# Kernel tuning notes

Hardware: AMD Instinct MI355X
Metric: run time of the kernel (lower is better)

Reference implementation:

```python
import math
import jax, jax.numpy as jnp
from jax import lax
import numpy as np

D_MODEL, D_STATE, D_CONV, EXPAND = 96, 16, 3, 2
D_INNER = EXPAND * D_MODEL            # 192
DT_RANK = math.ceil(D_MODEL / 16)     # 6
B_, H_, W_ = 2, 64, 64


def setup_inputs() -> dict:
    key = jax.random.key(0)
    ks = jax.random.split(key, 8)
    x = jax.random.normal(ks[0], (B_, H_, W_, D_MODEL), jnp.float32)
    in_proj_w = jax.random.normal(ks[1], (2 * D_INNER, D_MODEL), jnp.float32) * (D_MODEL ** -0.5)
    conv_w = jax.random.normal(ks[2], (D_INNER, 1, D_CONV, D_CONV), jnp.float32) * 0.1  # depthwise OIHW
    conv_b = jax.random.normal(ks[3], (D_INNER,), jnp.float32) * 0.1
    x_proj_weight = jax.random.normal(ks[4], (4, DT_RANK + 2 * D_STATE, D_INNER), jnp.float32) * (D_INNER ** -0.5)
    dt_init_std = DT_RANK ** -0.5
    dt_projs_weight = jax.random.uniform(ks[5], (4, D_INNER, DT_RANK), jnp.float32, -dt_init_std, dt_init_std)
    dt = jnp.exp(jax.random.uniform(ks[6], (4, D_INNER), jnp.float32) * (math.log(0.1) - math.log(0.001)) + math.log(0.001))
    dt = jnp.clip(dt, 1e-4, None)
    dt_projs_bias = dt + jnp.log(-jnp.expm1(-dt))  # inverse softplus init
    A_logs = jnp.log(jnp.tile(jnp.arange(1.0, D_STATE + 1.0, dtype=jnp.float32), (4 * D_INNER, 1)))  # (4*D, N)
    Ds = jnp.ones((4 * D_INNER,), jnp.float32)
    out_norm_w = jnp.ones((D_INNER,), jnp.float32)
    out_norm_b = jnp.zeros((D_INNER,), jnp.float32)
    out_proj_w = jax.random.normal(ks[7], (D_MODEL, D_INNER), jnp.float32) * (D_INNER ** -0.5)
    return dict(x=x, in_proj_w=in_proj_w, conv_w=conv_w, conv_b=conv_b,
                x_proj_weight=x_proj_weight, dt_projs_weight=dt_projs_weight,
                dt_projs_bias=dt_projs_bias, A_logs=A_logs, Ds=Ds,
                out_norm_w=out_norm_w, out_norm_b=out_norm_b, out_proj_w=out_proj_w)


def _ss2d(x, in_proj_w, conv_w, conv_b, x_proj_weight, dt_projs_weight,
          dt_projs_bias, A_logs, Ds, out_norm_w, out_norm_b, out_proj_w):
    B, H, W, C = x.shape
    K = 4
    d_inner = conv_w.shape[0]
    d_state = A_logs.shape[1]
    dt_rank = dt_projs_weight.shape[2]
    L = H * W

    # in_proj + split into x / gate z
    xz = jnp.einsum('bhwc,ec->bhwe', x, in_proj_w)
    xi, z = jnp.split(xz, 2, axis=-1)

    # depthwise 3x3 conv (padding=1) + SiLU, channels-first
    xc = jnp.transpose(xi, (0, 3, 1, 2))  # B,D,H,W
    xc = lax.conv_general_dilated(xc, conv_w, (1, 1), 'SAME',
                                  feature_group_count=d_inner,
                                  dimension_numbers=('NCHW', 'OIHW', 'NCHW'))
    xc = jax.nn.silu(xc + conv_b[None, :, None, None])

    # 4 scan directions: row-major, col-major, and their reverses
    x_hw = xc.reshape(B, d_inner, L)
    x_wh = jnp.transpose(xc, (0, 1, 3, 2)).reshape(B, d_inner, L)
    x_hwwh = jnp.stack([x_hw, x_wh], axis=1)                        # B,2,D,L
    xs = jnp.concatenate([x_hwwh, jnp.flip(x_hwwh, axis=-1)], axis=1)  # B,K,D,L

    x_dbl = jnp.einsum('bkdl,kcd->bkcl', xs, x_proj_weight)
    dts, Bs, Cs = jnp.split(x_dbl, [dt_rank, dt_rank + d_state], axis=2)
    dts = jnp.einsum('bkrl,kdr->bkdl', dts, dt_projs_weight)
    delta = jax.nn.softplus(dts + dt_projs_bias[None, :, :, None])  # B,K,D,L
    A = -jnp.exp(A_logs).reshape(K, d_inner, d_state)               # K,D,N

    # selective scan over L (serial recurrence)
    d_s = jnp.moveaxis(delta, -1, 0)  # L,B,K,D
    u_s = jnp.moveaxis(xs, -1, 0)     # L,B,K,D
    B_s = jnp.moveaxis(Bs, -1, 0)     # L,B,K,N
    C_s = jnp.moveaxis(Cs, -1, 0)     # L,B,K,N

    def step(h, inp):
        d_t, u_t, Bt, Ct = inp
        dA = jnp.exp(d_t[..., None] * A)                       # B,K,D,N
        h = h * dA + (d_t * u_t)[..., None] * Bt[:, :, None, :]
        y = jnp.einsum('bkdn,bkn->bkd', h, Ct)
        return h, y

    h0 = jnp.zeros((B, K, d_inner, d_state), jnp.float32)
    _, ys = lax.scan(step, h0, (d_s, u_s, B_s, C_s))  # ys: L,B,K,D
    ys = jnp.moveaxis(ys, 0, -1)                      # B,K,D,L
    out_y = ys + xs * Ds.reshape(K, d_inner)[None, :, :, None]

    # merge directions back to row-major layout
    inv_y = jnp.flip(out_y[:, 2:4], axis=-1)
    wh_y = jnp.transpose(out_y[:, 1].reshape(B, d_inner, W, H), (0, 1, 3, 2)).reshape(B, d_inner, L)
    invwh_y = jnp.transpose(inv_y[:, 1].reshape(B, d_inner, W, H), (0, 1, 3, 2)).reshape(B, d_inner, L)
    y = out_y[:, 0] + inv_y[:, 0] + wh_y + invwh_y    # B,D,L

    y = jnp.transpose(y, (0, 2, 1)).reshape(B, H, W, d_inner)
    mu = y.mean(-1, keepdims=True)
    var = y.var(-1, keepdims=True)
    y = (y - mu) * lax.rsqrt(var + 1e-5) * out_norm_w + out_norm_b
    y = y * jax.nn.silu(z)
    return jnp.einsum('bhwd,cd->bhwc', y, out_proj_w)


def reference(x, in_proj_w, conv_w, conv_b, x_proj_weight, dt_projs_weight,
              dt_projs_bias, A_logs, Ds, out_norm_w, out_norm_b, out_proj_w):
    return _ss2d(x, in_proj_w, conv_w, conv_b, x_proj_weight, dt_projs_weight,
                 dt_projs_bias, A_logs, Ds, out_norm_w, out_norm_b, out_proj_w)
```

## Files before the change

### kernel.cpp

```cpp
#include <hip/hip_runtime.h>
#include <math.h>

#define DMODEL 96
#define DIN    192
#define NST    16
#define RK     6
#define KDIR   4
#define LLEN   4096
#define BB     2
#define BP_TOT 8192
#define SCH    128
#define TCH    32

__global__ __launch_bounds__(192) void k_inproj(const float* __restrict__ x,
                                                const float* __restrict__ Wp,
                                                float* __restrict__ xi,
                                                float* __restrict__ z)
{
    __shared__ float xs[8 * 96];
    const int t  = threadIdx.x;
    const int p0 = blockIdx.x * 8;
    for (int idx = t; idx < 768; idx += 192)
        xs[idx] = x[(size_t)p0 * 96 + idx];
    __syncthreads();

    float acc0[8], acc1[8];
    #pragma unroll
    for (int i = 0; i < 8; ++i) { acc0[i] = 0.f; acc1[i] = 0.f; }
    const float* w0p = Wp + (size_t)t * 96;
    const float* w1p = Wp + (size_t)(t + 192) * 96;
    for (int k = 0; k < 96; k += 4) {
        float4 w0 = *(const float4*)(w0p + k);
        float4 w1 = *(const float4*)(w1p + k);
        #pragma unroll
        for (int p = 0; p < 8; ++p) {
            float4 xv = *(const float4*)&xs[p * 96 + k];
            acc0[p] = fmaf(w0.x, xv.x, fmaf(w0.y, xv.y, fmaf(w0.z, xv.z, fmaf(w0.w, xv.w, acc0[p]))));
            acc1[p] = fmaf(w1.x, xv.x, fmaf(w1.y, xv.y, fmaf(w1.z, xv.z, fmaf(w1.w, xv.w, acc1[p]))));
        }
    }
    #pragma unroll
    for (int p = 0; p < 8; ++p) {
        xi[(size_t)(p0 + p) * 192 + t] = acc0[p];
        z [(size_t)(p0 + p) * 192 + t] = acc1[p];
    }
}

__device__ __forceinline__ int inv_perm(int kd, int p)
{
    if (kd == 0) return p;
    if (kd == 1) return ((p & 63) << 6) | (p >> 6);
    if (kd == 2) return 4095 - p;
    return 4095 - (((p & 63) << 6) | (p >> 6));
}

__device__ __forceinline__ int perm_pos(int k, int l)
{
    if (k == 0) return l;
    if (k == 1) return ((l & 63) << 6) | (l >> 6);
    if (k == 2) return 4095 - l;
    int lr = 4095 - l;
    return ((lr & 63) << 6) | (lr >> 6);
}

__device__ __forceinline__ float softplus_fast(float x)
{
    float r = __logf(1.f + __expf(x));
    return (x > 15.f) ? x : r;
}

__device__ __forceinline__ void pow_chain(float e1, float* aa)
{
    float e2 = e1 * e1, e4 = e2 * e2, e8 = e4 * e4, e16 = e8 * e8;
    float e3 = e2 * e1, e5 = e4 * e1, e6 = e4 * e2, e7 = e4 * e3;
    aa[0] = e1;  aa[1] = e2;  aa[2] = e3;  aa[3] = e4;
    aa[4] = e5;  aa[5] = e6;  aa[6] = e7;  aa[7] = e8;
    aa[8] = e8 * e1;  aa[9] = e8 * e2;  aa[10] = e8 * e3;  aa[11] = e8 * e4;
    aa[12] = e8 * e5; aa[13] = e8 * e6; aa[14] = e8 * e7;  aa[15] = e16;
}

__device__ __forceinline__ int sm_remap(int c)
{
    return (c < 6) ? (32 + c) : (c - 6);
}

__global__ __launch_bounds__(192) void k_convxdbl(const float* __restrict__ xi,
                                                  const float* __restrict__ cw,
                                                  const float* __restrict__ cb,
                                                  const float* __restrict__ xpw,
                                                  float* __restrict__ xc,
                                                  float* __restrict__ xdk)
{
    __shared__ float xs[8 * 192];
    const int t   = threadIdx.x;
    const int p0  = blockIdx.x * 8;
    const int b   = p0 >> 12;
    const int pp0 = p0 & 4095;
    const int row = pp0 >> 6, c0 = pp0 & 63;

    float w9[9];
    #pragma unroll
    for (int i = 0; i < 9; ++i) w9[i] = cw[t * 9 + i];
    const float cbias = cb[t];

    float xv[3][10];
    #pragma unroll
    for (int ky = 0; ky < 3; ++ky) {
        int rr = row + ky - 1;
        #pragma unroll
        for (int kx = 0; kx < 10; ++kx) {
            int cc = c0 + kx - 1;
            float v = 0.f;
            if (rr >= 0 && rr < 64 && cc >= 0 && cc < 64)
                v = xi[((size_t)b * 4096 + rr * 64 + cc) * 192 + t];
            xv[ky][kx] = v;
        }
    }
    #pragma unroll
    for (int p = 0; p < 8; ++p) {
        float s = cbias;
        #pragma unroll
        for (int ky = 0; ky < 3; ++ky)
            #pragma unroll
            for (int kx = 0; kx < 3; ++kx)
                s = fmaf(xv[ky][p + kx], w9[ky * 3 + kx], s);
        float sv = s * (1.f / (1.f + __expf(-s)));
        xc[(size_t)(p0 + p) * 192 + t] = sv;
        xs[p * 192 + t] = sv;
    }
    __syncthreads();
    if (t >= 152) return;

    const int kd = t / 38, r = t % 38;
    float acc[8];
    #pragma unroll
    for (int i = 0; i < 8; ++i) acc[i] = 0.f;
    const float* wr = xpw + (size_t)t * 192;
    for (int k = 0; k < 192; k += 4) {
        float4 w = *(const float4*)(wr + k);
        #pragma unroll
        for (int p = 0; p < 8; ++p) {
            float4 x4 = *(const float4*)&xs[p * 192 + k];
            acc[p] = fmaf(w.x, x4.x, fmaf(w.y, x4.y, fmaf(w.z, x4.z, fmaf(w.w, x4.w, acc[p]))));
        }
    }
    #pragma unroll
    for (int p = 0; p < 8; ++p) {
        int pp = pp0 + p;
        int l  = inv_perm(kd, pp);
        xdk[((size_t)(b * 4 + kd) * 4096 + l) * 38 + r] = acc[p];
    }
}

__global__ __launch_bounds__(192) void k_scan1(const float* __restrict__ xc,
                                               const float* __restrict__ xdk,
                                               const float* __restrict__ dtw,
                                               const float* __restrict__ dtb,
                                               const float* __restrict__ Alog,
                                               float* __restrict__ hend,
                                               float* __restrict__ prodA)
{
    __shared__ float sm[TCH * 40];
    const int t   = threadIdx.x;
    const int blk = blockIdx.x;
    const int s = blk & (SCH - 1), k = (blk >> 7) & 3, b = blk >> 9;
    const int kd = k * 192 + t;
    const int l0 = s * TCH;

    const float* src = xdk + ((size_t)(b * 4 + k) * 4096 + l0) * 38;
    for (int idx = t; idx < TCH * 38; idx += 192) {
        int st = idx / 38, c = idx % 38;
        sm[st * 40 + sm_remap(c)] = src[idx];
    }

    const float A0 = -__expf(Alog[kd * 16]);
    bool fast = true;
    #pragma unroll
    for (int n = 1; n < 16; ++n) {
        float An = -__expf(Alog[kd * 16 + n]);
        fast = fast && (fabsf(An - (float)(n + 1) * A0) <= 1e-3f * fabsf(An));
    }
    float wdt[6];
    #pragma unroll
    for (int r = 0; r < 6; ++r) wdt[r] = dtw[kd * 6 + r];
    const float bias = dtb[kd];

    float h[16];
    #pragma unroll
    for (int n = 0; n < 16; ++n) h[n] = 0.f;
    float cd = 0.f;

    const float* xcb = xc + (size_t)b * 4096 * 192;
    int allfast = __syncthreads_and((int)fast);

    int p_cur = perm_pos(k, l0);
    float u = xcb[(size_t)p_cur * 192 + t];

    if (allfast) {
        for (int g0 = 0; g0 < TCH; g0 += 8) {
            float e18[8], dl8[8];
            #pragma unroll
            for (int j = 0; j < 8; ++j) {
                const float* r = &sm[(g0 + j) * 40];
                float4 dq = *(const float4*)(r + 32);
                float xv = bias + dq.x * wdt[0] + dq.y * wdt[1] + dq.z * wdt[2]
                                + dq.w * wdt[3] + r[36] * wdt[4] + r[37] * wdt[5];
                float delta = softplus_fast(xv);
                dl8[j] = delta;
                e18[j] = __expf(delta * A0);
            }
            #pragma unroll
            for (int j = 0; j < 8; ++j) {
                int st = g0 + j;
                int p_next = (st + 1 < TCH) ? perm_pos(k, l0 + st + 1) : p_cur;
                float u_next = xcb[(size_t)p_next * 192 + t];
                const float* r = &sm[st * 40];
                cd += dl8[j];
                float du = dl8[j] * u;
                float aa[16];
                pow_chain(e18[j], aa);
                float4 b0 = *(const float4*)(r),      b1 = *(const float4*)(r + 4);
                float4 b2 = *(const float4*)(r + 8),  b3 = *(const float4*)(r + 12);
                float bv[16] = {b0.x, b0.y, b0.z, b0.w, b1.x, b1.y, b1.z, b1.w,
                                b2.x, b2.y, b2.z, b2.w, b3.x, b3.y, b3.z, b3.w};
                #pragma unroll
                for (int n = 0; n < 16; ++n)
                    h[n] = fmaf(h[n], aa[n], du * bv[n]);
                u = u_next; p_cur = p_next;
            }
        }
    } else {
        for (int st = 0; st < TCH; ++st) {
            int p_next = (st + 1 < TCH) ? perm_pos(k, l0 + st + 1) : p_cur;
            float u_next = xcb[(size_t)p_next * 192 + t];
            const float* r = &sm[st * 40];
            float xv = bias;
            #pragma unroll
            for (int j = 0; j < 6; ++j) xv += r[32 + j] * wdt[j];
            float delta = softplus_fast(xv);
            cd += delta;
            float du = delta * u;
            #pragma unroll
            for (int n = 0; n < 16; ++n) {
                float An = -__expf(Alog[kd * 16 + n]);
                h[n] = fmaf(h[n], __expf(delta * An), du * r[n]);
            }
            u = u_next; p_cur = p_next;
        }
    }

    size_t base = (size_t)blk * 3072 + t * 16;
    float ap[16];
    if (allfast) {
        pow_chain(__expf(cd * A0), ap);
    } else {
        #pragma unroll
        for (int n = 0; n < 16; ++n)
            ap[n] = __expf(-__expf(Alog[kd * 16 + n]) * cd);
    }
    #pragma unroll
    for (int i = 0; i < 4; ++i) {
        *(float4*)&hend [base + 4 * i] = make_float4(h[4*i], h[4*i+1], h[4*i+2], h[4*i+3]);
        *(float4*)&prodA[base + 4 * i] = make_float4(ap[4*i], ap[4*i+1], ap[4*i+2], ap[4*i+3]);
    }
}

__global__ __launch_bounds__(256) void k_scan2(const float* __restrict__ hend,
                                               float* __restrict__ prodA)
{
    __shared__ float smA[256], smH[256];
    const int t = threadIdx.x;
    const int g = t >> 4, n = t & 15;
    const int bk = blockIdx.x / 192, d = blockIdx.x % 192;
    const size_t base = (size_t)bk * SCH * 3072 + d * 16 + n;

    float a_[8], h_[8];
    float A = 1.f, H = 0.f;
    #pragma unroll
    for (int i = 0; i < 8; ++i) {
        size_t rec = base + (size_t)(g * 8 + i) * 3072;
        a_[i] = prodA[rec];
        h_[i] = hend[rec];
        H = fmaf(a_[i], H, h_[i]);
        A *= a_[i];
    }
    smA[t] = A; smH[t] = H;
    __syncthreads();
    if (t < 16) {
        float carry = 0.f;
        for (int g2 = 0; g2 < 16; ++g2) {
            float ta = smA[g2 * 16 + t], th = smH[g2 * 16 + t];
            smH[g2 * 16 + t] = carry;
            carry = fmaf(ta, carry, th);
        }
    }
    __syncthreads();
    float carry = smH[t];
    #pragma unroll
    for (int i = 0; i < 8; ++i) {
        size_t rec = base + (size_t)(g * 8 + i) * 3072;
        prodA[rec] = carry;
        carry = fmaf(a_[i], carry, h_[i]);
    }
}

__global__ __launch_bounds__(192) void k_scan3(const float* __restrict__ xc,
                                               const float* __restrict__ xdk,
                                               const float* __restrict__ dtw,
                                               const float* __restrict__ dtb,
                                               const float* __restrict__ Alog,
                                               const float* __restrict__ Ds,
                                               const float* __restrict__ hinit,
                                               float* __restrict__ yk)
{
    __shared__ float sm[TCH * 40];
    const int t   = threadIdx.x;
    const int blk = blockIdx.x;
    const int s = blk & (SCH - 1), k = (blk >> 7) & 3, b = blk >> 9;
    const int kd = k * 192 + t;
    const int l0 = s * TCH;

    const float* src = xdk + ((size_t)(b * 4 + k) * 4096 + l0) * 38;
    float* ykb = yk + (size_t)(b * 4 + k) * 4096 * 192;

    for (int idx = t; idx < TCH * 38; idx += 192) {
        int st = idx / 38, c = idx % 38;
        sm[st * 40 + sm_remap(c)] = src[idx];
    }

    const float A0 = -__expf(Alog[kd * 16]);
    bool fast = true;
    #pragma unroll
    for (int n = 1; n < 16; ++n) {
        float An = -__expf(Alog[kd * 16 + n]);
        fast = fast && (fabsf(An - (float)(n + 1) * A0) <= 1e-3f * fabsf(An));
    }
    float wdt[6];
    #pragma unroll
    for (int r = 0; r < 6; ++r) wdt[r] = dtw[kd * 6 + r];
    const float bias = dtb[kd];
    const float Dk   = Ds[kd];

    float h[16];
    size_t hbase = (size_t)blk * 3072 + t * 16;
    #pragma unroll
    for (int i = 0; i < 4; ++i) {
        float4 v = *(const float4*)&hinit[hbase + 4 * i];
        h[4*i] = v.x; h[4*i+1] = v.y; h[4*i+2] = v.z; h[4*i+3] = v.w;
    }

    const float* xcb = xc + (size_t)b * 4096 * 192;
    int allfast = __syncthreads_and((int)fast);

    int p_cur = perm_pos(k, l0);
    float u = xcb[(size_t)p_cur * 192 + t];

    if (allfast) {
        for (int g0 = 0; g0 < TCH; g0 += 8) {
            float e18[8], dl8[8];
            #pragma unroll
            for (int j = 0; j < 8; ++j) {
                const float* r = &sm[(g0 + j) * 40];
                float4 dq = *(const float4*)(r + 32);
                float xv = bias + dq.x * wdt[0] + dq.y * wdt[1] + dq.z * wdt[2]
                                + dq.w * wdt[3] + r[36] * wdt[4] + r[37] * wdt[5];
                float delta = softplus_fast(xv);
                dl8[j] = delta;
                e18[j] = __expf(delta * A0);
            }
            #pragma unroll
            for (int j = 0; j < 8; ++j) {
                int st = g0 + j;
                int p_next = (st + 1 < TCH) ? perm_pos(k, l0 + st + 1) : p_cur;
                float u_next = xcb[(size_t)p_next * 192 + t];
                const float* r = &sm[st * 40];
                float du = dl8[j] * u;
                float aa[16];
                pow_chain(e18[j], aa);
                float4 b0 = *(const float4*)(r),      b1 = *(const float4*)(r + 4);
                float4 b2 = *(const float4*)(r + 8),  b3 = *(const float4*)(r + 12);
                float4 c0 = *(const float4*)(r + 16), c1 = *(const float4*)(r + 20);
                float4 c2 = *(const float4*)(r + 24), c3 = *(const float4*)(r + 28);
                float bv[16] = {b0.x, b0.y, b0.z, b0.w, b1.x, b1.y, b1.z, b1.w,
                                b2.x, b2.y, b2.z, b2.w, b3.x, b3.y, b3.z, b3.w};
                float cv[16] = {c0.x, c0.y, c0.z, c0.w, c1.x, c1.y, c1.z, c1.w,
                                c2.x, c2.y, c2.z, c2.w, c3.x, c3.y, c3.z, c3.w};
                float acc = Dk * u;
                #pragma unroll
                for (int n = 0; n < 16; ++n) {
                    h[n] = fmaf(h[n], aa[n], du * bv[n]);
                    acc  = fmaf(h[n], cv[n], acc);
                }
                ykb[(size_t)p_cur * 192 + t] = acc;
                u = u_next; p_cur = p_next;
            }
        }
    } else {
        for (int st = 0; st < TCH; ++st) {
            int p_next = (st + 1 < TCH) ? perm_pos(k, l0 + st + 1) : p_cur;
            float u_next = xcb[(size_t)p_next * 192 + t];
            const float* r = &sm[st * 40];
            float xv = bias;
            #pragma unroll
            for (int j = 0; j < 6; ++j) xv += r[32 + j] * wdt[j];
            float delta = softplus_fast(xv);
            float du = delta * u;
            float acc = Dk * u;
            #pragma unroll
            for (int n = 0; n < 16; ++n) {
                float An = -__expf(Alog[kd * 16 + n]);
                h[n] = fmaf(h[n], __expf(delta * An), du * r[n]);
                acc  = fmaf(h[n], r[16 + n], acc);
            }
            ykb[(size_t)p_cur * 192 + t] = acc;
            u = u_next; p_cur = p_next;
        }
    }
}

__global__ __launch_bounds__(192) void k_lnout(const float* __restrict__ yk,
                                               const float* __restrict__ zb,
                                               const float* __restrict__ onw,
                                               const float* __restrict__ onb,
                                               const float* __restrict__ Wo,
                                               float* __restrict__ out)
{
    __shared__ float ys[1536];
    __shared__ float ps[192], pq[192];
    __shared__ float mu[8], ri[8];
    const int t   = threadIdx.x;
    const int p0  = blockIdx.x * 8;
    const int b   = p0 >> 12;
    const int pp0 = p0 & 4095;
    const size_t KSTR = (size_t)4096 * 192;

    #pragma unroll
    for (int i = 0; i < 8; ++i) {
        size_t base = ((size_t)(b * 4) * 4096 + pp0 + i) * 192 + t;
        ys[i * 192 + t] = yk[base] + yk[base + KSTR] + yk[base + 2 * KSTR] + yk[base + 3 * KSTR];
    }
    __syncthreads();

    {
        int pg = t / 24, j = t % 24;
        float s1 = 0.f, s2 = 0.f;
        #pragma unroll
        for (int m = 0; m < 8; ++m) {
            float v = ys[pg * 192 + j + 24 * m];
            s1 += v; s2 += v * v;
        }
        ps[t] = s1; pq[t] = s2;
    }
    __syncthreads();
    if (t < 8) {
        float s1 = 0.f, s2 = 0.f;
        #pragma unroll
        for (int j = 0; j < 24; ++j) { s1 += ps[t * 24 + j]; s2 += pq[t * 24 + j]; }
        float mean = s1 * (1.f / 192.f);
        float var  = s2 * (1.f / 192.f) - mean * mean;
        mu[t] = mean;
        ri[t] = rsqrtf(var + 1e-5f);
    }
    __syncthreads();

    {
        float w = onw[t], bo = onb[t];
        #pragma unroll
        for (int i = 0; i < 8; ++i) {
            float v  = ys[i * 192 + t];
            float yn = (v - mu[i]) * ri[i] * w + bo;
            float zv = zb[(size_t)(p0 + i) * 192 + t];
            float sg = 1.f / (1.f + __expf(-zv));
            ys[i * 192 + t] = yn * (zv * sg);
        }
    }
    __syncthreads();

    const int pg = t / 96, c = t % 96;
    float acc[4];
    #pragma unroll
    for (int i = 0; i < 4; ++i) acc[i] = 0.f;
    const float* wr = Wo + (size_t)c * 192;
    for (int k = 0; k < 192; k += 4) {
        float4 w = *(const float4*)(wr + k);
        #pragma unroll
        for (int i = 0; i < 4; ++i) {
            float4 xv = *(const float4*)&ys[(pg * 4 + i) * 192 + k];
            acc[i] = fmaf(w.x, xv.x, fmaf(w.y, xv.y, fmaf(w.z, xv.z, fmaf(w.w, xv.w, acc[i]))));
        }
    }
    #pragma unroll
    for (int i = 0; i < 4; ++i)
        out[(size_t)(p0 + pg * 4 + i) * 96 + c] = acc[i];
}

extern "C" void kernel_launch(void* const* d_in, const int* in_sizes, int n_in,
                              void* d_out, int out_size, void* d_ws, size_t ws_size,
                              hipStream_t stream)
{
    const float* x    = (const float*)d_in[0];
    const float* Wp   = (const float*)d_in[1];
    const float* cw   = (const float*)d_in[2];
    const float* cb   = (const float*)d_in[3];
    const float* xpw  = (const float*)d_in[4];
    const float* dtw  = (const float*)d_in[5];
    const float* dtb  = (const float*)d_in[6];
    const float* Alog = (const float*)d_in[7];
    const float* Ds   = (const float*)d_in[8];
    const float* onw  = (const float*)d_in[9];
    const float* onb  = (const float*)d_in[10];
    const float* Wo   = (const float*)d_in[11];
    float* out = (float*)d_out;

    const size_t NBP  = (size_t)BP_TOT * 192;
    const size_t NXD  = (size_t)BB * 4 * 4096 * 38;
    const size_t NSC  = (size_t)BB * 4 * SCH * 3072;
    float* WS    = (float*)d_ws;
    float* xibuf = WS;
    float* zb    = WS + NBP;
    float* xc    = WS + 2 * NBP;
    float* xdk   = WS + 3 * NBP;
    float* hend  = xdk + NXD;
    float* prodA = hend + NSC;
    float* yk    = prodA + NSC;

    k_inproj  <<<1024, 192, 0, stream>>>(x, Wp, xibuf, zb);
    k_convxdbl<<<1024, 192, 0, stream>>>(xibuf, cw, cb, xpw, xc, xdk);
    k_scan1   <<<1024, 192, 0, stream>>>(xc, xdk, dtw, dtb, Alog, hend, prodA);
    k_scan2   <<<1536, 256, 0, stream>>>(hend, prodA);
    k_scan3   <<<1024, 192, 0, stream>>>(xc, xdk, dtw, dtb, Alog, Ds, prodA, yk);
    k_lnout   <<<1024, 192, 0, stream>>>(yk, zb, onw, onb, Wo, out);
}
```

Baseline: 214.5 us.

## Preload scan inputs into shared memory and compress chunk decay products

Result: faster. 201.3 us (-6.2%).

```diff
diff --git a/kernel.cpp b/kernel.cpp
--- a/kernel.cpp
+++ b/kernel.cpp
@@ -63,6 +63,11 @@
     return ((lr & 63) << 6) | (lr >> 6);
 }
 
+__device__ __forceinline__ int perm_dir(int k)
+{
+    return (k == 0) ? 1 : (k == 1) ? 64 : (k == 2) ? -1 : -64;
+}
+
 __device__ __forceinline__ float softplus_fast(float x)
 {
     float r = __logf(1.f + __expf(x));
@@ -79,6 +84,18 @@
     aa[12] = e8 * e5; aa[13] = e8 * e6; aa[14] = e8 * e7;  aa[15] = e16;
 }
 
+__device__ __forceinline__ float pow_n(float W, int e)
+{
+    float w2 = W * W, w4 = w2 * w2, w8 = w4 * w4;
+    float r = 1.f;
+    if (e & 1) r *= W;
+    if (e & 2) r *= w2;
+    if (e & 4) r *= w4;
+    if (e & 8) r *= w8;
+    if (e & 16) r = w8 * w8;
+    return r;
+}
+
 __device__ __forceinline__ int sm_remap(int c)
 {
     return (c < 6) ? (32 + c) : (c - 6);
@@ -158,20 +175,28 @@
                                                const float* __restrict__ dtb,
                                                const float* __restrict__ Alog,
                                                float* __restrict__ hend,
-                                               float* __restrict__ prodA)
+                                               float* __restrict__ prodA,
+                                               float* __restrict__ Wbuf)
 {
     __shared__ float sm[TCH * 40];
+    __shared__ float su[TCH * 192];
     const int t   = threadIdx.x;
     const int blk = blockIdx.x;
     const int s = blk & (SCH - 1), k = (blk >> 7) & 3, b = blk >> 9;
     const int kd = k * 192 + t;
     const int l0 = s * TCH;
+    const int pstart = perm_pos(k, l0);
+    const int dir    = perm_dir(k);
 
     const float* src = xdk + ((size_t)(b * 4 + k) * 4096 + l0) * 38;
     for (int idx = t; idx < TCH * 38; idx += 192) {
         int st = idx / 38, c = idx % 38;
         sm[st * 40 + sm_remap(c)] = src[idx];
     }
+    const float* xcb = xc + (size_t)b * 4096 * 192;
+    #pragma unroll
+    for (int i = 0; i < TCH; ++i)
+        su[i * 192 + t] = xcb[(size_t)(pstart + i * dir) * 192 + t];
 
     const float A0 = -__expf(Alog[kd * 16]);
     bool fast = true;
@@ -190,50 +215,33 @@
     for (int n = 0; n < 16; ++n) h[n] = 0.f;
     float cd = 0.f;
 
-    const float* xcb = xc + (size_t)b * 4096 * 192;
-    int allfast = __syncthreads_and((int)fast);
-
-    int p_cur = perm_pos(k, l0);
-    float u = xcb[(size_t)p_cur * 192 + t];
-
-    if (allfast) {
-        for (int g0 = 0; g0 < TCH; g0 += 8) {
-            float e18[8], dl8[8];
-            #pragma unroll
-            for (int j = 0; j < 8; ++j) {
-                const float* r = &sm[(g0 + j) * 40];
-                float4 dq = *(const float4*)(r + 32);
-                float xv = bias + dq.x * wdt[0] + dq.y * wdt[1] + dq.z * wdt[2]
-                                + dq.w * wdt[3] + r[36] * wdt[4] + r[37] * wdt[5];
-                float delta = softplus_fast(xv);
-                dl8[j] = delta;
-                e18[j] = __expf(delta * A0);
-            }
-            #pragma unroll
-            for (int j = 0; j < 8; ++j) {
-                int st = g0 + j;
-                int p_next = (st + 1 < TCH) ? perm_pos(k, l0 + st + 1) : p_cur;
-                float u_next = xcb[(size_t)p_next * 192 + t];
-                const float* r = &sm[st * 40];
-                cd += dl8[j];
-                float du = dl8[j] * u;
-                float aa[16];
-                pow_chain(e18[j], aa);
-                float4 b0 = *(const float4*)(r),      b1 = *(const float4*)(r + 4);
-                float4 b2 = *(const float4*)(r + 8),  b3 = *(const float4*)(r + 12);
-                float bv[16] = {b0.x, b0.y, b0.z, b0.w, b1.x, b1.y, b1.z, b1.w,
-                                b2.x, b2.y, b2.z, b2.w, b3.x, b3.y, b3.z, b3.w};
-                #pragma unroll
-                for (int n = 0; n < 16; ++n)
-                    h[n] = fmaf(h[n], aa[n], du * bv[n]);
-                u = u_next; p_cur = p_next;
-            }
-        }
+    __syncthreads();
+
+    if (fast) {
+        for (int st = 0; st < TCH; ++st) {
+            const float* r = &sm[st * 40];
+            float u = su[st * 192 + t];
+            float4 dq = *(const float4*)(r + 32);
+            float xv = bias + dq.x * wdt[0] + dq.y * wdt[1] + dq.z * wdt[2]
+                            + dq.w * wdt[3] + r[36] * wdt[4] + r[37] * wdt[5];
+            float delta = softplus_fast(xv);
+            cd += delta;
+            float du = delta * u;
+            float aa[16];
+            pow_chain(__expf(delta * A0), aa);
+            float4 b0 = *(const float4*)(r),      b1 = *(const float4*)(r + 4);
+            float4 b2 = *(const float4*)(r + 8),  b3 = *(const float4*)(r + 12);
+            float bv[16] = {b0.x, b0.y, b0.z, b0.w, b1.x, b1.y, b1.z, b1.w,
+                            b2.x, b2.y, b2.z, b2.w, b3.x, b3.y, b3.z, b3.w};
+            #pragma unroll
+            for (int n = 0; n < 16; ++n)
+                h[n] = fmaf(h[n], aa[n], du * bv[n]);
+        }
+        Wbuf[(size_t)blk * 192 + t] = __expf(cd * A0);
     } else {
         for (int st = 0; st < TCH; ++st) {
-            int p_next = (st + 1 < TCH) ? perm_pos(k, l0 + st + 1) : p_cur;
-            float u_next = xcb[(size_t)p_next * 192 + t];
             const float* r = &sm[st * 40];
+            float u = su[st * 192 + t];
             float xv = bias;
             #pragma unroll
             for (int j = 0; j < 6; ++j) xv += r[32 + j] * wdt[j];
@@ -245,44 +253,56 @@
                 float An = -__expf(Alog[kd * 16 + n]);
                 h[n] = fmaf(h[n], __expf(delta * An), du * r[n]);
             }
-            u = u_next; p_cur = p_next;
-        }
+        }
+        size_t base = (size_t)blk * 3072 + t * 16;
+        #pragma unroll
+        for (int n = 0; n < 16; ++n)
+            prodA[base + n] = __expf(-__expf(Alog[kd * 16 + n]) * cd);
     }
 
     size_t base = (size_t)blk * 3072 + t * 16;
-    float ap[16];
-    if (allfast) {
-        pow_chain(__expf(cd * A0), ap);
-    } else {
-        #pragma unroll
-        for (int n = 0; n < 16; ++n)
-            ap[n] = __expf(-__expf(Alog[kd * 16 + n]) * cd);
-    }
-    #pragma unroll
-    for (int i = 0; i < 4; ++i) {
-        *(float4*)&hend [base + 4 * i] = make_float4(h[4*i], h[4*i+1], h[4*i+2], h[4*i+3]);
-        *(float4*)&prodA[base + 4 * i] = make_float4(ap[4*i], ap[4*i+1], ap[4*i+2], ap[4*i+3]);
-    }
+    #pragma unroll
+    for (int i = 0; i < 4; ++i)
+        *(float4*)&hend[base + 4 * i] = make_float4(h[4*i], h[4*i+1], h[4*i+2], h[4*i+3]);
 }
 
 __global__ __launch_bounds__(256) void k_scan2(const float* __restrict__ hend,
-                                               float* __restrict__ prodA)
+                                               float* __restrict__ prodA,
+                                               const float* __restrict__ Wbuf,
+                                               const float* __restrict__ Alog)
 {
     __shared__ float smA[256], smH[256];
     const int t = threadIdx.x;
     const int g = t >> 4, n = t & 15;
     const int bk = blockIdx.x / 192, d = blockIdx.x % 192;
+    const int kd = (bk & 3) * 192 + d;
     const size_t base = (size_t)bk * SCH * 3072 + d * 16 + n;
+
+    const float A0 = -__expf(Alog[kd * 16]);
+    bool fast = true;
+    #pragma unroll
+    for (int m = 1; m < 16; ++m) {
+        float An = -__expf(Alog[kd * 16 + m]);
+        fast = fast && (fabsf(An - (float)(m + 1) * A0) <= 1e-3f * fabsf(An));
+    }
 
     float a_[8], h_[8];
     float A = 1.f, H = 0.f;
     #pragma unroll
     for (int i = 0; i < 8; ++i) {
-        size_t rec = base + (size_t)(g * 8 + i) * 3072;
-        a_[i] = prodA[rec];
+        int s = g * 8 + i;
+        size_t rec = base + (size_t)s * 3072;
+        float ai;
+        if (fast) {
+            float W = Wbuf[((size_t)bk * SCH + s) * 192 + d];
+            ai = pow_n(W, n + 1);
+        } else {
+            ai = prodA[rec];
+        }
+        a_[i] = ai;
         h_[i] = hend[rec];
-        H = fmaf(a_[i], H, h_[i]);
-        A *= a_[i];
+        H = fmaf(ai, H, h_[i]);
+        A *= ai;
     }
     smA[t] = A; smH[t] = H;
     __syncthreads();
@@ -314,19 +334,24 @@
                                                float* __restrict__ yk)
 {
     __shared__ float sm[TCH * 40];
+    __shared__ float su[TCH * 192];
     const int t   = threadIdx.x;
     const int blk = blockIdx.x;
     const int s = blk & (SCH - 1), k = (blk >> 7) & 3, b = blk >> 9;
     const int kd = k * 192 + t;
     const int l0 = s * TCH;
+    const int pstart = perm_pos(k, l0);
+    const int dir    = perm_dir(k);
 
     const float* src = xdk + ((size_t)(b * 4 + k) * 4096 + l0) * 38;
-    float* ykb = yk + (size_t)(b * 4 + k) * 4096 * 192;
-
     for (int idx = t; idx < TCH * 38; idx += 192) {
         int st = idx / 38, c = idx % 38;
         sm[st * 40 + sm_remap(c)] = src[idx];
     }
+    const float* xcb = xc + (size_t)b * 4096 * 192;
+    #pragma unroll
+    for (int i = 0; i < TCH; ++i)
+        su[i * 192 + t] = xcb[(size_t)(pstart + i * dir) * 192 + t];
 
     const float A0 = -__expf(Alog[kd * 16]);
     bool fast = true;
@@ -349,57 +374,43 @@
         h[4*i] = v.x; h[4*i+1] = v.y; h[4*i+2] = v.z; h[4*i+3] = v.w;
     }
 
-    const float* xcb = xc + (size_t)b * 4096 * 192;
-    int allfast = __syncthreads_and((int)fast);
-
-    int p_cur = perm_pos(k, l0);
-    float u = xcb[(size_t)p_cur * 192 + t];
-
-    if (allfast) {
-        for (int g0 = 0; g0 < TCH; g0 += 8) {
-            float e18[8], dl8[8];
-            #pragma unroll
-            for (int j = 0; j < 8; ++j) {
-                const float* r = &sm[(g0 + j) * 40];
-                float4 dq = *(const float4*)(r + 32);
-                float xv = bias + dq.x * wdt[0] + dq.y * wdt[1] + dq.z * wdt[2]
-                                + dq.w * wdt[3] + r[36] * wdt[4] + r[37] * wdt[5];
-                float delta = softplus_fast(xv);
-                dl8[j] = delta;
-                e18[j] = __expf(delta * A0);
+    float* yp = yk + (size_t)(b * 4 + k) * 4096 * 192 + (size_t)pstart * 192 + t;
+    const int ystep = dir * 192;
+
+    __syncthreads();
+
+    if (fast) {
+        for (int st = 0; st < TCH; ++st) {
+            const float* r = &sm[st * 40];
+            float u = su[st * 192 + t];
+            float4 dq = *(const float4*)(r + 32);
+            float xv = bias + dq.x * wdt[0] + dq.y * wdt[1] + dq.z * wdt[2]
+                            + dq.w * wdt[3] + r[36] * wdt[4] + r[37] * wdt[5];
+            float delta = softplus_fast(xv);
+            float du = delta * u;
+            float aa[16];
+            pow_chain(__expf(delta * A0), aa);
+            float4 b0 = *(const float4*)(r),      b1 = *(const float4*)(r + 4);
+            float4 b2 = *(const float4*)(r + 8),  b3 = *(const float4*)(r + 12);
+            float4 c0 = *(const float4*)(r + 16), c1 = *(const float4*)(r + 20);
+            float4 c2 = *(const float4*)(r + 24), c3 = *(const float4*)(r + 28);
+            float bv[16] = {b0.x, b0.y, b0.z, b0.w, b1.x, b1.y, b1.z, b1.w,
+                            b2.x, b2.y, b2.z, b2.w, b3.x, b3.y, b3.z, b3.w};
+            float cv[16] = {c0.x, c0.y, c0.z, c0.w, c1.x, c1.y, c1.z, c1.w,
+                            c2.x, c2.y, c2.z, c2.w, c3.x, c3.y, c3.z, c3.w};
+            float acc = Dk * u;
+            #pragma unroll
+            for (int n = 0; n < 16; ++n) {
+                h[n] = fmaf(h[n], aa[n], du * bv[n]);
+                acc  = fmaf(h[n], cv[n], acc);
             }
-            #pragma unroll
-            for (int j = 0; j < 8; ++j) {
-                int st = g0 + j;
-                int p_next = (st + 1 < TCH) ? perm_pos(k, l0 + st + 1) : p_cur;
-                float u_next = xcb[(size_t)p_next * 192 + t];
-                const float* r = &sm[st * 40];
-                float du = dl8[j] * u;
-                float aa[16];
-                pow_chain(e18[j], aa);
-                float4 b0 = *(const float4*)(r),      b1 = *(const float4*)(r + 4);
-                float4 b2 = *(const float4*)(r + 8),  b3 = *(const float4*)(r + 12);
-                float4 c0 = *(const float4*)(r + 16), c1 = *(const float4*)(r + 20);
-                float4 c2 = *(const float4*)(r + 24), c3 = *(const float4*)(r + 28);
-                float bv[16] = {b0.x, b0.y, b0.z, b0.w, b1.x, b1.y, b1.z, b1.w,
-                                b2.x, b2.y, b2.z, b2.w, b3.x, b3.y, b3.z, b3.w};
-                float cv[16] = {c0.x, c0.y, c0.z, c0.w, c1.x, c1.y, c1.z, c1.w,
-                                c2.x, c2.y, c2.z, c2.w, c3.x, c3.y, c3.z, c3.w};
-                float acc = Dk * u;
-                #pragma unroll
-                for (int n = 0; n < 16; ++n) {
-                    h[n] = fmaf(h[n], aa[n], du * bv[n]);
-                    acc  = fmaf(h[n], cv[n], acc);
-                }
-                ykb[(size_t)p_cur * 192 + t] = acc;
-                u = u_next; p_cur = p_next;
-            }
+            *yp = acc;
+            yp += ystep;
         }
     } else {
         for (int st = 0; st < TCH; ++st) {
-            int p_next = (st + 1 < TCH) ? perm_pos(k, l0 + st + 1) : p_cur;
-            float u_next = xcb[(size_t)p_next * 192 + t];
             const float* r = &sm[st * 40];
+            float u = su[st * 192 + t];
             float xv = bias;
             #pragma unroll
             for (int j = 0; j < 6; ++j) xv += r[32 + j] * wdt[j];
@@ -412,8 +423,8 @@
                 h[n] = fmaf(h[n], __expf(delta * An), du * r[n]);
                 acc  = fmaf(h[n], r[16 + n], acc);
             }
-            ykb[(size_t)p_cur * 192 + t] = acc;
-            u = u_next; p_cur = p_next;
+            *yp = acc;
+            yp += ystep;
         }
     }
 }
@@ -515,6 +526,7 @@
     const size_t NBP  = (size_t)BP_TOT * 192;
     const size_t NXD  = (size_t)BB * 4 * 4096 * 38;
     const size_t NSC  = (size_t)BB * 4 * SCH * 3072;
+    const size_t NW   = (size_t)BB * 4 * SCH * 192;
     float* WS    = (float*)d_ws;
     float* xibuf = WS;
     float* zb    = WS + NBP;
@@ -522,12 +534,13 @@
     float* xdk   = WS + 3 * NBP;
     float* hend  = xdk + NXD;
     float* prodA = hend + NSC;
-    float* yk    = prodA + NSC;
+    float* Wbuf  = prodA + NSC;
+    float* yk    = Wbuf + NW;
 
     k_inproj  <<<1024, 192, 0, stream>>>(x, Wp, xibuf, zb);
     k_convxdbl<<<1024, 192, 0, stream>>>(xibuf, cw, cb, xpw, xc, xdk);
-    k_scan1   <<<1024, 192, 0, stream>>>(xc, xdk, dtw, dtb, Alog, hend, prodA);
-    k_scan2   <<<1536, 256, 0, stream>>>(hend, prodA);
+    k_scan1   <<<1024, 192, 0, stream>>>(xc, xdk, dtw, dtb, Alog, hend, prodA, Wbuf);
+    k_scan2   <<<1536, 256, 0, stream>>>(hend, prodA, Wbuf, Alog);
     k_scan3   <<<1024, 192, 0, stream>>>(xc, xdk, dtw, dtb, Alog, Ds, prodA, yk);
     k_lnout   <<<1024, 192, 0, stream>>>(yk, zb, onw, onb, Wo, out);
 }
```
